# Kernel optimization log

Measured on AMD Instinct MI355X. Metric: run time of the kernel, lower is better.

The kernel has to match this reference:

```python
import jax, jax.numpy as jnp
import numpy as np

IN, HID, BATCH = 1024, 1024, 4096


def _linear_params(key, out_dim, in_dim):
    # torch.nn.Linear default init: U(-1/sqrt(in), 1/sqrt(in))
    k1, k2 = jax.random.split(key)
    bound = 1.0 / np.sqrt(in_dim)
    w = jax.random.uniform(k1, (out_dim, in_dim), jnp.float32, -bound, bound)
    b = jax.random.uniform(k2, (out_dim,), jnp.float32, -bound, bound)
    return w, b


def setup_inputs() -> dict:
    key = jax.random.key(0)
    keys = jax.random.split(key, 11)
    inp = {
        'input': jax.random.normal(keys[0], (BATCH, IN), jnp.float32),
        'h': jax.random.normal(keys[1], (BATCH, HID), jnp.float32),
        'c': jax.random.normal(keys[2], (BATCH, HID), jnp.float32),
    }
    names = ['i_i', 'i_h', 'f_i', 'f_h', 'g_i', 'g_h', 'o_i', 'o_h']
    for n, k in zip(names, keys[3:]):
        in_dim = IN if n.endswith('_i') else HID
        w, b = _linear_params(k, HID, in_dim)
        inp['w_' + n] = w
        inp['b_' + n] = b
    return inp


def reference(input, h, c,
              w_i_i, b_i_i, w_i_h, b_i_h,
              w_f_i, b_f_i, w_f_h, b_f_h,
              w_g_i, b_g_i, w_g_h, b_g_h,
              w_o_i, b_o_i, w_o_h, b_o_h):
    def lin(x, w, b):
        return x @ w.T + b

    i = jax.nn.sigmoid(lin(input, w_i_i, b_i_i) + lin(h, w_i_h, b_i_h))
    f = jax.nn.sigmoid(lin(input, w_f_i, b_f_i) + lin(h, w_f_h, b_f_h))
    g = jnp.tanh(lin(input, w_g_i, b_g_i) + lin(h, w_g_h, b_g_h))
    o = jax.nn.sigmoid(lin(input, w_o_i, b_o_i) + lin(h, w_o_h, b_o_h))
    c_prime = f * c + i * g
    h_prime = o * jnp.tanh(c_prime)
    return (h_prime, c_prime)
```

## Files before the change

### kernel.cpp

```cpp
#include <hip/hip_runtime.h>
#include <stdint.h>

#define BATCH 4096
#define IN_DIM 1024
#define HID 1024
#define KDIM 2048
#define NGATE 4096
#define EPITCH 136
#define BK 64
#define BM 256
#define BN 128

typedef __attribute__((ext_vector_type(4))) float floatx4;
typedef __attribute__((ext_vector_type(8))) __bf16 bf16x8;
typedef __attribute__((ext_vector_type(8))) unsigned short ushort8;

__device__ __forceinline__ unsigned short f2bf(float f) {
    union { float f; unsigned int u; } v; v.f = f;
    unsigned int u = v.u;
    u += 0x7fffu + ((u >> 16) & 1u);
    return (unsigned short)(u >> 16);
}
__device__ __forceinline__ float bf2f(unsigned short s) {
    union { unsigned int u; float f; } v; v.u = ((unsigned int)s) << 16;
    return v.f;
}
__device__ __forceinline__ ushort8 cvt8(const float* __restrict__ src) {
    float4 v0 = ((const float4*)src)[0];
    float4 v1 = ((const float4*)src)[1];
    ushort8 o = { f2bf(v0.x), f2bf(v0.y), f2bf(v0.z), f2bf(v0.w),
                  f2bf(v1.x), f2bf(v1.y), f2bf(v1.z), f2bf(v1.w) };
    return o;
}

__global__ __launch_bounds__(256) void prep_kernel(
    const float* __restrict__ x,  const float* __restrict__ h,
    const float* __restrict__ wii, const float* __restrict__ wih,
    const float* __restrict__ wfi, const float* __restrict__ wfh,
    const float* __restrict__ wgi, const float* __restrict__ wgh,
    const float* __restrict__ woi, const float* __restrict__ woh,
    const float* __restrict__ bii, const float* __restrict__ bih,
    const float* __restrict__ bfi, const float* __restrict__ bfh,
    const float* __restrict__ bgi, const float* __restrict__ bgh,
    const float* __restrict__ boi, const float* __restrict__ boh,
    unsigned short* __restrict__ Xb,
    unsigned short* __restrict__ Wb,
    float* __restrict__ bias)
{
    const int bid = blockIdx.x;
    const int tid = threadIdx.x;

    if (bid < 2048) {
        const int e = (bid * 256 + tid) * 8;
        const int b = e >> 10, k = e & 1023;
        *(ushort8*)(Xb + (size_t)b * KDIM + k) = cvt8(x + e);
    } else if (bid < 4096) {
        const int e = ((bid - 2048) * 256 + tid) * 8;
        const int b = e >> 10, k = e & 1023;
        *(ushort8*)(Xb + (size_t)b * KDIM + 1024 + k) = cvt8(h + e);
    } else if (bid < 8192) {
        const int m   = (bid - 4096) >> 9;
        const int off = (bid - 4096) & 511;
        const int e = (off * 256 + tid) * 8;
        const int n = e >> 10, k = e & 1023;
        const float* src;
        switch (m) {
            case 0: src = wii; break; case 1: src = wih; break;
            case 2: src = wfi; break; case 3: src = wfh; break;
            case 4: src = wgi; break; case 5: src = wgh; break;
            case 6: src = woi; break; default: src = woh; break;
        }
        const int gate = m >> 1, part = m & 1;
        *(ushort8*)(Wb + (size_t)(n * 4 + gate) * KDIM + part * 1024 + k)
            = cvt8(src + e);
    } else {
        const int t = (bid - 8192) * 256 + tid;
        const int gate = (bid - 8192) >> 2;
        const int n = t & 1023;
        const float *bi, *bh_;
        switch (gate) {
            case 0: bi = bii; bh_ = bih; break;
            case 1: bi = bfi; bh_ = bfh; break;
            case 2: bi = bgi; bh_ = bgh; break;
            default: bi = boi; bh_ = boh; break;
        }
        bias[n * 4 + gate] = bi[n] + bh_[n];
    }
}

#define GLD16(g, l)                                                          \
    __builtin_amdgcn_global_load_lds(                                        \
        (__attribute__((address_space(1))) void*)(g),                        \
        (__attribute__((address_space(3))) void*)(l), 16, 0, 0)

__global__ __launch_bounds__(512) void gemm_lstm(
    const unsigned short* __restrict__ X,
    const unsigned short* __restrict__ W,
    const float* __restrict__ bias,
    const float* __restrict__ c_in,
    float* __restrict__ out)
{
    __shared__ __align__(16) unsigned char smem[49152];
    unsigned short* As = (unsigned short*)smem;
    unsigned short* Bs = (unsigned short*)(smem + 32768);
    unsigned short* E  = (unsigned short*)smem;

    const int tid  = threadIdx.x;
    const int wave = tid >> 6;
    const int lane = tid & 63;
    const int quad = lane >> 4, idx = lane & 15;
    const int wm = (wave >> 1) * 64;
    const int wn = (wave & 1) * 64;

    const int l   = blockIdx.x;
    const int xcd = l & 7;
    const int s   = l >> 3;
    const int bx  = xcd * 2 + (s >> 5);
    const int by  = s & 31;
    const int rowA0 = bx * BM;
    const int rowB0 = by * BN;

    const int srow = tid >> 3;
    const int skk  = ((tid & 7) ^ (srow & 7)) * 8;
    const unsigned short* gA = X + (size_t)(rowA0 + srow) * KDIM + skk;
    const unsigned short* gB = W + (size_t)(rowB0 + srow) * KDIM + skk;
    const size_t rstride = (size_t)64 * KDIM;

    const int swz = (idx & 7);

    floatx4 acc[4][4] = {};

    for (int k0 = 0; k0 < KDIM; k0 += BK) {
#pragma unroll
        for (int r = 0; r < 4; ++r)
            GLD16(gA + k0 + r * rstride, As + (r * 512 + tid) * 8);
#pragma unroll
        for (int r = 0; r < 2; ++r)
            GLD16(gB + k0 + r * rstride, Bs + (r * 512 + tid) * 8);
        __syncthreads();

        bf16x8 af[4][2], bfr[4][2];
#pragma unroll
        for (int t = 0; t < 2; ++t) {
            const int co = ((t * 4 + quad) ^ swz) * 8;
#pragma unroll
            for (int i = 0; i < 4; ++i)
                af[i][t] = *(const bf16x8*)(As + (wm + i * 16 + idx) * BK + co);
#pragma unroll
            for (int j = 0; j < 4; ++j)
                bfr[j][t] = *(const bf16x8*)(Bs + (wn + j * 16 + idx) * BK + co);
        }
#pragma unroll
        for (int t = 0; t < 2; ++t)
#pragma unroll
            for (int i = 0; i < 4; ++i)
#pragma unroll
                for (int j = 0; j < 4; ++j)
                    acc[i][j] = __builtin_amdgcn_mfma_f32_16x16x32_bf16(
                        af[i][t], bfr[j][t], acc[i][j], 0, 0, 0);
        __syncthreads();
    }

    const int g = idx & 3;
    const int tid8 = tid & 7;
    const int rowo = tid >> 3;
    float* __restrict__ out_h = out;
    float* __restrict__ out_c = out + (size_t)BATCH * HID;

#pragma unroll
    for (int half = 0; half < 2; ++half) {
        if ((wave >> 2) == half) {
            const int wml = wm - half * 128;
#pragma unroll
            for (int j = 0; j < 4; ++j) {
                const int col = wn + j * 16 + idx;
                const float bv = bias[rowB0 + col];
#pragma unroll
                for (int i = 0; i < 4; ++i) {
#pragma unroll
                    for (int r = 0; r < 4; ++r) {
                        const int row = wml + i * 16 + quad * 4 + r;
                        const float v  = acc[i][j][r] + bv;
                        const float vv = (g == 2) ? 2.f * v : v;
                        const float s2 = 1.f / (1.f + __expf(-vv));
                        const float a  = (g == 2) ? 2.f * s2 - 1.f : s2;
                        E[row * EPITCH + col] = f2bf(a);
                    }
                }
            }
        }
        __syncthreads();

#pragma unroll
        for (int p = 0; p < 2; ++p) {
            const int row_l = p * 64 + rowo;
            const int row_g = rowA0 + half * 128 + row_l;
            const int colc  = tid8 * 16;
            ushort8 e0 = *(const ushort8*)(E + row_l * EPITCH + colc);
            ushort8 e1 = *(const ushort8*)(E + row_l * EPITCH + colc + 8);
            const int u0 = (rowB0 >> 2) + tid8 * 4;
            const float4 cv = *(const float4*)(c_in + (size_t)row_g * HID + u0);

            float cvv[4] = { cv.x, cv.y, cv.z, cv.w };
            float hp[4], cp[4];
#pragma unroll
            for (int d = 0; d < 4; ++d) {
                const ushort8& e = (d < 2) ? e0 : e1;
                const int b = (d & 1) * 4;
                const float iv = bf2f(e[b + 0]);
                const float fv = bf2f(e[b + 1]);
                const float gv = bf2f(e[b + 2]);
                const float ov = bf2f(e[b + 3]);
                const float c2 = fv * cvv[d] + iv * gv;
                const float e2 = __expf(2.f * c2);
                cp[d] = c2;
                hp[d] = ov * ((e2 - 1.f) / (e2 + 1.f));
            }
            float4 hv  = { hp[0], hp[1], hp[2], hp[3] };
            float4 cpv = { cp[0], cp[1], cp[2], cp[3] };
            *(float4*)(out_h + (size_t)row_g * HID + u0) = hv;
            *(float4*)(out_c + (size_t)row_g * HID + u0) = cpv;
        }
        __syncthreads();
    }
}

extern "C" void kernel_launch(void* const* d_in, const int* in_sizes, int n_in,
                              void* d_out, int out_size, void* d_ws, size_t ws_size,
                              hipStream_t stream) {
    const float* x   = (const float*)d_in[0];
    const float* h   = (const float*)d_in[1];
    const float* c   = (const float*)d_in[2];
    const float* wii = (const float*)d_in[3];
    const float* bii = (const float*)d_in[4];
    const float* wih = (const float*)d_in[5];
    const float* bih = (const float*)d_in[6];
    const float* wfi = (const float*)d_in[7];
    const float* bfi = (const float*)d_in[8];
    const float* wfh = (const float*)d_in[9];
    const float* bfh = (const float*)d_in[10];
    const float* wgi = (const float*)d_in[11];
    const float* bgi = (const float*)d_in[12];
    const float* wgh = (const float*)d_in[13];
    const float* bgh = (const float*)d_in[14];
    const float* woi = (const float*)d_in[15];
    const float* boi = (const float*)d_in[16];
    const float* woh = (const float*)d_in[17];
    const float* boh = (const float*)d_in[18];

    char* ws = (char*)d_ws;
    unsigned short* Xb  = (unsigned short*)ws;
    unsigned short* Wb  = (unsigned short*)(ws + ((size_t)16 << 20));
    float*          bsv = (float*)(ws + ((size_t)32 << 20));

    prep_kernel<<<8208, 256, 0, stream>>>(
        x, h, wii, wih, wfi, wfh, wgi, wgh, woi, woh,
        bii, bih, bfi, bfh, bgi, bgh, boi, boh, Xb, Wb, bsv);

    gemm_lstm<<<(BATCH / BM) * (NGATE / BN), 512, 0, stream>>>(
        Xb, Wb, bsv, c, (float*)d_out);
}
```

Baseline: 210.9 us.

## Enlarge GEMM tile to 256x256 with double-buffered, phase-interleaved LDS pipeline

Grows the output tile from 256x128 to 256x256 and splits each K-step into quarter sub-tiles in 128 KB of LDS, split into two buffers. Global-to-LDS loads for upcoming k-steps are issued while MFMA runs on the current quarter, using explicit vmcnt waits, raw s_barrier and s_setprio. The aim is to hide load latency behind compute and raise arithmetic intensity. In exchange it uses far more LDS and registers, launch_bounds(512,2) may not be reachable with that LDS, and the epilogue is reworked for the wider tile.

```diff
diff --git a/kernel.cpp b/kernel.cpp
--- a/kernel.cpp
+++ b/kernel.cpp
@@ -6,10 +6,11 @@
 #define HID 1024
 #define KDIM 2048
 #define NGATE 4096
-#define EPITCH 136
 #define BK 64
 #define BM 256
-#define BN 128
+#define BN 256
+#define NT (KDIM / BK)
+#define EPITCH2 264
 
 typedef __attribute__((ext_vector_type(4))) float floatx4;
 typedef __attribute__((ext_vector_type(8))) __bf16 bf16x8;
@@ -92,31 +93,40 @@
     __builtin_amdgcn_global_load_lds(                                        \
         (__attribute__((address_space(1))) void*)(g),                        \
         (__attribute__((address_space(3))) void*)(l), 16, 0, 0)
-
-__global__ __launch_bounds__(512) void gemm_lstm(
+#define BAR()     asm volatile("s_barrier" ::: "memory")
+#define VMCNT(n)  asm volatile("s_waitcnt vmcnt(" #n ")" ::: "memory")
+
+__global__ __launch_bounds__(512, 2) void gemm_lstm(
     const unsigned short* __restrict__ X,
     const unsigned short* __restrict__ W,
     const float* __restrict__ bias,
     const float* __restrict__ c_in,
     float* __restrict__ out)
 {
-    __shared__ __align__(16) unsigned char smem[49152];
-    unsigned short* As = (unsigned short*)smem;
-    unsigned short* Bs = (unsigned short*)(smem + 32768);
-    unsigned short* E  = (unsigned short*)smem;
+    __shared__ __align__(16) unsigned char smem[131072];
+    unsigned short* sA[2][2];
+    unsigned short* sB[2][2];
+#pragma unroll
+    for (int b_ = 0; b_ < 2; ++b_)
+#pragma unroll
+        for (int h_ = 0; h_ < 2; ++h_) {
+            sA[b_][h_] = (unsigned short*)(smem + ((b_ * 2 + h_) << 14));
+            sB[b_][h_] = (unsigned short*)(smem + 65536 + ((b_ * 2 + h_) << 14));
+        }
 
     const int tid  = threadIdx.x;
     const int wave = tid >> 6;
     const int lane = tid & 63;
-    const int quad = lane >> 4, idx = lane & 15;
-    const int wm = (wave >> 1) * 64;
-    const int wn = (wave & 1) * 64;
+    const int idx  = lane & 15;
+    const int quad = lane >> 4;
+    const int wrow = wave >> 2;
+    const int wcol = wave & 3;
 
     const int l   = blockIdx.x;
     const int xcd = l & 7;
     const int s   = l >> 3;
-    const int bx  = xcd * 2 + (s >> 5);
-    const int by  = s & 31;
+    const int bx  = xcd * 2 + (s >> 4);
+    const int by  = s & 15;
     const int rowA0 = bx * BM;
     const int rowB0 = by * BN;
 
@@ -124,67 +134,106 @@
     const int skk  = ((tid & 7) ^ (srow & 7)) * 8;
     const unsigned short* gA = X + (size_t)(rowA0 + srow) * KDIM + skk;
     const unsigned short* gB = W + (size_t)(rowB0 + srow) * KDIM + skk;
-    const size_t rstride = (size_t)64 * KDIM;
-
-    const int swz = (idx & 7);
-
-    floatx4 acc[4][4] = {};
-
-    for (int k0 = 0; k0 < KDIM; k0 += BK) {
-#pragma unroll
-        for (int r = 0; r < 4; ++r)
-            GLD16(gA + k0 + r * rstride, As + (r * 512 + tid) * 8);
-#pragma unroll
-        for (int r = 0; r < 2; ++r)
-            GLD16(gB + k0 + r * rstride, Bs + (r * 512 + tid) * 8);
-        __syncthreads();
-
-        bf16x8 af[4][2], bfr[4][2];
-#pragma unroll
-        for (int t = 0; t < 2; ++t) {
-            const int co = ((t * 4 + quad) ^ swz) * 8;
-#pragma unroll
-            for (int i = 0; i < 4; ++i)
-                af[i][t] = *(const bf16x8*)(As + (wm + i * 16 + idx) * BK + co);
-#pragma unroll
-            for (int j = 0; j < 4; ++j)
-                bfr[j][t] = *(const bf16x8*)(Bs + (wn + j * 16 + idx) * BK + co);
-        }
-#pragma unroll
-        for (int t = 0; t < 2; ++t)
-#pragma unroll
-            for (int i = 0; i < 4; ++i)
-#pragma unroll
-                for (int j = 0; j < 4; ++j)
-                    acc[i][j] = __builtin_amdgcn_mfma_f32_16x16x32_bf16(
-                        af[i][t], bfr[j][t], acc[i][j], 0, 0, 0);
-        __syncthreads();
+
+#define STAGE_A(buf, ht, kt) do {                                             \
+    GLD16(gA + ((size_t)((ht) * 128)) * KDIM + (size_t)(kt) * 64,             \
+          sA[buf][ht] + tid * 8);                                             \
+    GLD16(gA + ((size_t)((ht) * 128 + 64)) * KDIM + (size_t)(kt) * 64,        \
+          sA[buf][ht] + 4096 + tid * 8);                                      \
+  } while (0)
+#define STAGE_B(buf, ht, kt) do {                                             \
+    GLD16(gB + ((size_t)((ht) * 128)) * KDIM + (size_t)(kt) * 64,             \
+          sB[buf][ht] + tid * 8);                                             \
+    GLD16(gB + ((size_t)((ht) * 128 + 64)) * KDIM + (size_t)(kt) * 64,        \
+          sB[buf][ht] + 4096 + tid * 8);                                      \
+  } while (0)
+
+    const int aoff = (wrow * 64 + idx) * 64;
+    const int boff = (wcol * 32 + idx) * 64;
+    const int co0  = (quad ^ (idx & 7)) * 8;
+    const int co1  = ((4 + quad) ^ (idx & 7)) * 8;
+
+    bf16x8 af[4][2], bfr[2][2];
+    floatx4 acc[2][2][4][2] = {};
+
+#define RD_A(buf, MH) do {                                                    \
+    const unsigned short* pA_ = sA[buf][MH] + aoff;                           \
+    _Pragma("unroll") for (int i_ = 0; i_ < 4; ++i_) {                        \
+        af[i_][0] = *(const bf16x8*)(pA_ + i_ * 1024 + co0);                  \
+        af[i_][1] = *(const bf16x8*)(pA_ + i_ * 1024 + co1); }                \
+  } while (0)
+#define RD_B(buf, NH) do {                                                    \
+    const unsigned short* pB_ = sB[buf][NH] + boff;                           \
+    _Pragma("unroll") for (int j_ = 0; j_ < 2; ++j_) {                        \
+        bfr[j_][0] = *(const bf16x8*)(pB_ + j_ * 1024 + co0);                 \
+        bfr[j_][1] = *(const bf16x8*)(pB_ + j_ * 1024 + co1); }               \
+  } while (0)
+#define MM(MH, NH) do {                                                       \
+    __builtin_amdgcn_s_setprio(1);                                            \
+    _Pragma("unroll") for (int i_ = 0; i_ < 4; ++i_)                          \
+    _Pragma("unroll") for (int j_ = 0; j_ < 2; ++j_) {                        \
+        acc[MH][NH][i_][j_] = __builtin_amdgcn_mfma_f32_16x16x32_bf16(        \
+            af[i_][0], bfr[j_][0], acc[MH][NH][i_][j_], 0, 0, 0);             \
+        acc[MH][NH][i_][j_] = __builtin_amdgcn_mfma_f32_16x16x32_bf16(        \
+            af[i_][1], bfr[j_][1], acc[MH][NH][i_][j_], 0, 0, 0); }           \
+    __builtin_amdgcn_s_setprio(0);                                            \
+  } while (0)
+
+    STAGE_A(0, 0, 0); STAGE_B(0, 0, 0); STAGE_B(0, 1, 0); STAGE_A(0, 1, 0);
+    STAGE_A(1, 0, 1); STAGE_B(1, 1, 1); STAGE_A(1, 1, 1);
+    VMCNT(6);
+    BAR();
+
+    for (int t0 = 0; t0 < NT - 2; t0 += 2) {
+        const int t1 = t0 + 1;
+        RD_A(0, 0); RD_B(0, 0); STAGE_B(1, 0, t1);     BAR(); MM(0, 0); BAR();
+        RD_B(0, 1);             STAGE_A(0, 0, t0 + 2); BAR(); MM(0, 1); BAR();
+        RD_A(0, 1);             STAGE_B(0, 1, t0 + 2); BAR(); MM(1, 1); BAR();
+        RD_B(0, 0);             STAGE_A(0, 1, t0 + 2); VMCNT(6);
+                                                       BAR(); MM(1, 0); BAR();
+        RD_A(1, 0); RD_B(1, 0); STAGE_B(0, 0, t0 + 2); BAR(); MM(0, 0); BAR();
+        RD_B(1, 1);             STAGE_A(1, 0, t1 + 2); BAR(); MM(0, 1); BAR();
+        RD_A(1, 1);             STAGE_B(1, 1, t1 + 2); BAR(); MM(1, 1); BAR();
+        RD_B(1, 0);             STAGE_A(1, 1, t1 + 2); VMCNT(6);
+                                                       BAR(); MM(1, 0); BAR();
     }
-
-    const int g = idx & 3;
-    const int tid8 = tid & 7;
-    const int rowo = tid >> 3;
+    {
+        RD_A(0, 0); RD_B(0, 0); STAGE_B(1, 0, NT - 1); BAR(); MM(0, 0); BAR();
+        RD_B(0, 1);                                    BAR(); MM(0, 1); BAR();
+        RD_A(0, 1);                                    BAR(); MM(1, 1); BAR();
+        RD_B(0, 0);             VMCNT(0);              BAR(); MM(1, 0); BAR();
+        RD_A(1, 0); RD_B(1, 0);                        BAR(); MM(0, 0); BAR();
+        RD_B(1, 1);                                    BAR(); MM(0, 1); BAR();
+        RD_A(1, 1);                                    BAR(); MM(1, 1); BAR();
+        RD_B(1, 0);                                    BAR(); MM(1, 0); BAR();
+    }
+
+    unsigned short* E = (unsigned short*)smem;
+    const int gate   = idx & 3;
+    const int rowo16 = tid >> 4;
+    const int t16    = tid & 15;
     float* __restrict__ out_h = out;
     float* __restrict__ out_c = out + (size_t)BATCH * HID;
 
 #pragma unroll
     for (int half = 0; half < 2; ++half) {
-        if ((wave >> 2) == half) {
-            const int wml = wm - half * 128;
-#pragma unroll
-            for (int j = 0; j < 4; ++j) {
-                const int col = wn + j * 16 + idx;
+#pragma unroll
+        for (int nh = 0; nh < 2; ++nh) {
+#pragma unroll
+            for (int j = 0; j < 2; ++j) {
+                const int col = nh * 128 + wcol * 32 + j * 16 + idx;
                 const float bv = bias[rowB0 + col];
 #pragma unroll
                 for (int i = 0; i < 4; ++i) {
 #pragma unroll
                     for (int r = 0; r < 4; ++r) {
-                        const int row = wml + i * 16 + quad * 4 + r;
-                        const float v  = acc[i][j][r] + bv;
-                        const float vv = (g == 2) ? 2.f * v : v;
+                        const int row = wrow * 64 + i * 16 + quad * 4 + r;
+                        const float v = ((half == 0) ? acc[0][nh][i][j][r]
+                                                     : acc[1][nh][i][j][r]) + bv;
+                        const float vv = (gate == 2) ? 2.f * v : v;
                         const float s2 = 1.f / (1.f + __expf(-vv));
-                        const float a  = (g == 2) ? 2.f * s2 - 1.f : s2;
-                        E[row * EPITCH + col] = f2bf(a);
+                        const float a  = (gate == 2) ? 2.f * s2 - 1.f : s2;
+                        E[row * EPITCH2 + col] = f2bf(a);
                     }
                 }
             }
@@ -192,13 +241,13 @@
         __syncthreads();
 
 #pragma unroll
-        for (int p = 0; p < 2; ++p) {
-            const int row_l = p * 64 + rowo;
+        for (int p = 0; p < 4; ++p) {
+            const int row_l = p * 32 + rowo16;
             const int row_g = rowA0 + half * 128 + row_l;
-            const int colc  = tid8 * 16;
-            ushort8 e0 = *(const ushort8*)(E + row_l * EPITCH + colc);
-            ushort8 e1 = *(const ushort8*)(E + row_l * EPITCH + colc + 8);
-            const int u0 = (rowB0 >> 2) + tid8 * 4;
+            const int colc  = t16 * 16;
+            ushort8 e0 = *(const ushort8*)(E + row_l * EPITCH2 + colc);
+            ushort8 e1 = *(const ushort8*)(E + row_l * EPITCH2 + colc + 8);
+            const int u0 = (rowB0 >> 2) + t16 * 4;
             const float4 cv = *(const float4*)(c_in + (size_t)row_g * HID + u0);
 
             float cvv[4] = { cv.x, cv.y, cv.z, cv.w };
```

Result: no change. 215.1 us (+2.0%).
